# Optimization experiments

Measured on AMD Instinct MI355X. Metric: run time of the kernel, lower is better.

## Reference

```python
import jax, jax.numpy as jnp
import numpy as np

B, C, N, K = 2, 128, 8192, 16
DL = 128  # dim_L; Fourier half-dim = 64; mlp hidden = 32


def setup_inputs() -> dict:
    key = jax.random.key(0)
    ks = jax.random.split(key, 16)
    s = 0.05
    return {
        "x": jax.random.normal(ks[0], (B, C, N, 1), jnp.float32),
        "coords": jax.random.normal(ks[1], (B, N, 4), jnp.float32),
        "idx": jax.random.randint(ks[2], (B, N, K), 0, N, jnp.int64),
        "B_gauss": jax.random.normal(ks[3], (4, DL // 2), jnp.float32),
        "W1": jax.random.normal(ks[4], (DL, DL // 4), jnp.float32) * s,
        "b1": jax.random.normal(ks[5], (DL // 4,), jnp.float32) * s,
        "W2": jax.random.normal(ks[6], (DL // 4, C), jnp.float32) * s,
        "b2": jax.random.normal(ks[7], (C,), jnp.float32) * s,
        "Wq": jax.random.normal(ks[8], (C, C), jnp.float32) * s,
        "bq": jax.random.normal(ks[9], (C,), jnp.float32) * s,
        "Wk": jax.random.normal(ks[10], (C, C), jnp.float32) * s,
        "bk": jax.random.normal(ks[11], (C,), jnp.float32) * s,
        "Wv": jax.random.normal(ks[12], (C, C), jnp.float32) * s,
        "bv": jax.random.normal(ks[13], (C,), jnp.float32) * s,
        "Wo": jax.random.normal(ks[14], (C, C), jnp.float32) * s,
        "bo": jax.random.normal(ks[15], (C,), jnp.float32) * s,
    }


def reference(x, coords, idx, B_gauss, W1, b1, W2, b2, Wq, bq, Wk, bk, Wv, bv, Wo, bo):
    xs = x[..., 0]  # [B, C, N]
    # gather neighbor coords/features via KNN idx (vmapped over batch)
    nb_coords = jax.vmap(lambda c, i: c[i])(coords, idx)          # [B, N, K, 4]
    nb_feats = jax.vmap(lambda f, i: f[:, i])(xs, idx)            # [B, C, N, K]
    delta_p = nb_coords - coords[:, :, None, :]                   # [B, N, K, 4]
    # random-Fourier geometric embedding
    proj = jnp.matmul(delta_p, B_gauss)                           # [B, N, K, DL/2]
    two_pi = 2.0 * jnp.pi
    E_freq = jnp.concatenate([jnp.sin(two_pi * proj), jnp.cos(two_pi * proj)], axis=-1)
    h = jax.nn.relu(E_freq @ W1 + b1) @ W2 + b2                   # [B, N, K, C]
    E_geo = jnp.transpose(h, (0, 3, 1, 2))                        # [B, C, N, K]
    # 1x1 conv projections == channel matmuls (PyTorch conv weight acts as out<-in)
    Q = jnp.einsum('oc,bcn->bon', Wq, xs) + bq[None, :, None]     # [B, C, N]
    KV_in = nb_feats + E_geo                                      # [B, C, N, K]
    Kt = jnp.einsum('oc,bcnk->bonk', Wk, KV_in) + bk[None, :, None, None]
    Vt = jnp.einsum('oc,bcnk->bonk', Wv, KV_in) + bv[None, :, None, None]
    # local dot-product attention over K neighbors
    attn = jnp.sum(Q[..., None] * Kt, axis=1, keepdims=True) / jnp.sqrt(jnp.float32(C))
    attn = jax.nn.softmax(attn, axis=-1)                          # [B, 1, N, K]
    out = jnp.sum(attn * Vt, axis=-1, keepdims=True)              # [B, C, N, 1]
    out = jnp.einsum('oc,bcnk->bonk', Wo, out) + bo[None, :, None, None]
    return out
```

## Files before the change

### kernel.cpp

```cpp
#include <hip/hip_runtime.h>


using u16 = unsigned short;
using u32 = unsigned int;
using u64 = unsigned long long;

typedef short bf16x8 __attribute__((ext_vector_type(8)));
typedef float f32x4  __attribute__((ext_vector_type(4)));

__device__ __forceinline__ float bl(u32 u) { return __uint_as_float(u << 16); }
__device__ __forceinline__ float bh(u32 u) { return __uint_as_float(u & 0xffff0000u); }
__device__ __forceinline__ float b2f(u16 u) { return __uint_as_float(((u32)u) << 16); }
__device__ __forceinline__ u16 f2b(float f) {
    u32 u = __float_as_uint(f);
    u32 r = u + 0x7fffu + ((u >> 16) & 1u);
    return (u16)(r >> 16);
}
__device__ __forceinline__ float dot8(uint4 wv, const float* xp) {
    float4 a = *(const float4*)xp;
    float4 b = *(const float4*)(xp + 4);
    return bl(wv.x)*a.x + bh(wv.x)*a.y + bl(wv.y)*a.z + bh(wv.y)*a.w
         + bl(wv.z)*b.x + bh(wv.z)*b.y + bl(wv.w)*b.z + bh(wv.w)*b.w;
}
__device__ __forceinline__ u64 pack4(float a, float b, float c, float d) {
    return (u64)f2b(a) | ((u64)f2b(b) << 16) | ((u64)f2b(c) << 32) | ((u64)f2b(d) << 48);
}
__device__ __forceinline__ int fidxA(int m, int c) {
    return (((m >> 4)*4 + (c >> 5))*64 + ((c >> 3) & 3)*16 + (m & 15))*8 + (c & 7);
}

__global__ void __launch_bounds__(512)
k_pt(const float* __restrict__ x,
     const float* __restrict__ Wq, const float* __restrict__ bq,
     const float* __restrict__ Wk, const float* __restrict__ bk,
     const float* __restrict__ Wv, const float* __restrict__ bv,
     const float* __restrict__ Wo, const float* __restrict__ bo,
     const float* __restrict__ W1, const float* __restrict__ W2,
     const float* __restrict__ b2,
     u16* __restrict__ Afrag, u16* __restrict__ Wovfrag,
     u16* __restrict__ W1frag, u16* __restrict__ W2frag,
     u16* __restrict__ Wovt2frag,
     float* __restrict__ bA, float* __restrict__ su2,
     float* __restrict__ bov2, float* __restrict__ d0b,
     u16* __restrict__ xT)
{
    const int blk = blockIdx.x, tid = threadIdx.x;

    if (blk >= 130) {
        __shared__ u16 tile[32][33];
        const int blk2 = blk - 130;
        const int b  = blk2 >> 10;
        const int ct = (blk2 >> 8) & 3;
        const int nt = blk2 & 255;
        const int tx = tid & 31, ty = tid >> 5;
        const size_t xb = (size_t)b * 128 * 8192;
        #pragma unroll
        for (int j = 0; j < 2; ++j) {
            int c = ct*32 + ty + j*16;
            tile[ty + j*16][tx] = f2b(x[xb + (size_t)c * 8192 + (size_t)(nt*32 + tx)]);
        }
        __syncthreads();
        #pragma unroll
        for (int j = 0; j < 2; ++j) {
            int n = nt*32 + ty + j*16;
            xT[xb + (size_t)n * 128 + (size_t)(ct*32 + tx)] = tile[tx][ty + j*16];
        }
        return;
    }

    const int i = tid & 127, p = tid >> 7;
    if (blk < 128) {
        __shared__ float sWk[128], sWo[128];
        __shared__ float s_pA[4][128], s_pV[4][128];
        __shared__ float s_row[128];
        if (tid < 128) sWk[tid] = Wk[tid*128 + blk];
        else if (tid < 256) sWo[tid-128] = Wo[blk*128 + (tid-128)];
        __syncthreads();
        float accA = 0.f, accV = 0.f;
        #pragma unroll 8
        for (int o = p*32; o < p*32 + 32; ++o) {
            accA += sWk[o] * Wq[o*128 + i];
            accV += sWo[o] * Wv[o*128 + i];
        }
        s_pA[p][i] = accA; s_pV[p][i] = accV;
        __syncthreads();
        if (tid < 128) {
            float v = s_pA[0][tid] + s_pA[1][tid] + s_pA[2][tid] + s_pA[3][tid];
            Afrag[fidxA(blk, tid)] = f2b(v);
        } else if (tid < 256) {
            int ii = tid - 128;
            float v = s_pV[0][ii] + s_pV[1][ii] + s_pV[2][ii] + s_pV[3][ii];
            Wovfrag[fidxA(blk, ii)] = f2b(v);
            s_row[ii] = v;
        }
        __syncthreads();
        if (tid < 32) {
            float wv2 = 0.f;
            for (int c = 0; c < 128; ++c) wv2 += s_row[c] * W2[tid*128 + c];
            Wovt2frag[(((blk >> 4)*64) + (tid >> 3)*16 + (blk & 15))*8 + (tid & 7)] = f2b(wv2);
        } else if (tid == 32) {
            float rb2 = 0.f, a3 = 0.f;
            for (int c = 0; c < 128; ++c) rb2 += s_row[c] * b2[c];
            for (int o = 0; o < 128; ++o) a3 += sWo[o] * bv[o];
            bov2[blk] = rb2 + a3 + bo[blk];
        }
    } else if (blk == 128) {
        __shared__ float s_t[128];
        __shared__ float s_p1[4][128], s_p2[4][128];
        if (tid < 128) {
            float tt = 0.f;
            for (int c = 0; c < 128; ++c) tt += Wk[tid*128 + c] * b2[c];
            s_t[tid] = tt + bk[tid];
        }
        __syncthreads();
        float a1 = 0.f, a2 = 0.f;
        #pragma unroll 8
        for (int o = p*32; o < p*32 + 32; ++o) {
            a1 += Wk[o*128 + i] * bq[o];
            a2 += Wq[o*128 + i] * s_t[o];
        }
        s_p1[p][i] = a1; s_p2[p][i] = a2;
        __syncthreads();
        if (tid < 128) {
            bA[tid] = s_p1[0][tid] + s_p1[1][tid] + s_p1[2][tid] + s_p1[3][tid];
        } else if (tid < 256) {
            int ii = tid - 128;
            su2[ii] = s_p2[0][ii] + s_p2[1][ii] + s_p2[2][ii] + s_p2[3][ii];
        } else if (tid < 320) {
            int l = tid - 256;
            float part = bq[l]*s_t[l] + bq[l+64]*s_t[l+64];
            part += __shfl_xor(part, 1);
            part += __shfl_xor(part, 2);
            part += __shfl_xor(part, 4);
            part += __shfl_xor(part, 8);
            part += __shfl_xor(part, 16);
            part += __shfl_xor(part, 32);
            if (l == 0) *d0b = part;
        }
    } else {
        for (int e = tid; e < 4096; e += 512) {
            int ii = e & 127, r2 = e >> 7;
            {
                int nt = r2 >> 4, lmm = r2 & 15;
                int ks = ii >> 5, q = (ii >> 3) & 3, j = ii & 7;
                W1frag[((nt*4 + ks)*64 + q*16 + lmm)*8 + j] = f2b(W1[ii*32 + r2]);
            }
            {
                int mt = r2 >> 4, lmm = r2 & 15;
                int ks = ii >> 5, q = (ii >> 3) & 3, j = ii & 7;
                W2frag[((mt*4 + ks)*64 + q*16 + lmm)*8 + j] = f2b(W2[r2*128 + ii]);
            }
        }
    }
}

__global__ void __launch_bounds__(256)
k_main(const u16* __restrict__ xT, const float* __restrict__ coords,
       const int* __restrict__ idx, const float* __restrict__ Bg,
       const float* __restrict__ b1g,
       const u16* __restrict__ Afrag, const u16* __restrict__ Wovfrag,
       const u16* __restrict__ W1frag, const u16* __restrict__ W2frag,
       const u16* __restrict__ Wovt2frag,
       const float* __restrict__ bAg, const float* __restrict__ su2g,
       const float* __restrict__ bov2g, const float* __restrict__ d0bg,
       float* __restrict__ out)
{
    __shared__ __align__(16) u16   sH[128][84];
    __shared__ __align__(16) u16   s_qkb[8][136];
    __shared__ __align__(16) u16   s_gb[8][40];
    __shared__ __align__(16) u16   s_xb[8][136];
    __shared__ __align__(16) u16   sHbarT[8][40];
    __shared__ float s_attn[8][17];
    __shared__ float s_e0[8];
    __shared__ __align__(16) float sBgT[64][4];
    __shared__ int s_idx[128];

    const int tid = threadIdx.x;
    const int w = tid >> 6, l = tid & 63, lm = l & 15, lq = l >> 4, lmm = lm & 7;
    const int bsel = blockIdx.x & 1;
    const int n0 = (blockIdx.x >> 1) * 8;
    const int g0 = (bsel << 13) + n0;
    const size_t bbase = ((size_t)bsel) << 13;
    const float inv_sqrtC = 0.08838834764831845f;

    sBgT[tid >> 2][tid & 3] = Bg[(tid & 3)*64 + (tid >> 2)];
    const float c_d0b = *d0bg;

    const int r0 = (w*2)*16 + lm, r1 = (w*2 + 1)*16 + lm;
    const int j0 = idx[(size_t)g0*16 + r0];
    const int j1 = idx[(size_t)g0*16 + r1];
    if (lq == 0) { s_idx[r0] = j0; s_idx[r1] = j1; }
    float4 dA, dB;
    {
        float4 cj0 = *(const float4*)&coords[(size_t)(bbase + j0)*4];
        float4 cn0 = *(const float4*)&coords[(size_t)(g0 + w*2)*4];
        dA = make_float4(cj0.x-cn0.x, cj0.y-cn0.y, cj0.z-cn0.z, cj0.w-cn0.w);
        float4 cj1 = *(const float4*)&coords[(size_t)(bbase + j1)*4];
        float4 cn1 = *(const float4*)&coords[(size_t)(g0 + w*2 + 1)*4];
        dB = make_float4(cj1.x-cn1.x, cj1.y-cn1.y, cj1.z-cn1.z, cj1.w-cn1.w);
    }
    f32x4 accq[2] = {{0.f,0.f,0.f,0.f},{0.f,0.f,0.f,0.f}};
    {
        const bf16x8* Af = (const bf16x8*)Afrag;
        bf16x8 bfr[4];
        #pragma unroll
        for (int ks = 0; ks < 4; ++ks)
            bfr[ks] = *(const bf16x8*)&xT[(((size_t)(g0 + lmm)) << 7) + ks*32 + lq*8];
        #pragma unroll
        for (int mi = 0; mi < 2; ++mi) {
            const int ct = w*2 + mi;
            #pragma unroll
            for (int ks = 0; ks < 4; ++ks)
                accq[mi] = __builtin_amdgcn_mfma_f32_16x16x32_bf16(Af[(ct*4 + ks)*64 + l], bfr[ks], accq[mi], 0, 0, 0);
        }
    }
    if (tid >= 128 && tid < 192) {
        int t = tid - 128, n = t >> 3, sub = t & 7, c0 = sub*16;
        uint4 x0 = *(const uint4*)&xT[(((size_t)(g0 + n)) << 7) + c0];
        uint4 x1 = *(const uint4*)&xT[(((size_t)(g0 + n)) << 7) + c0 + 8];
        float part = dot8(x0, &su2g[c0]) + dot8(x1, &su2g[c0+8]);
        part += __shfl_xor(part, 1);
        part += __shfl_xor(part, 2);
        part += __shfl_xor(part, 4);
        if (sub == 0) s_e0[n] = part + c_d0b;
    }
    if (lm < 8) {
        #pragma unroll
        for (int mi = 0; mi < 2; ++mi) {
            int c0 = (w*2 + mi)*16 + lq*4;
            float4 bA4 = *(const float4*)&bAg[c0];
            *(u64*)&s_qkb[lm][c0] = pack4(accq[mi][0] + bA4.x, accq[mi][1] + bA4.y,
                                          accq[mi][2] + bA4.z, accq[mi][3] + bA4.w);
        }
    }
    __syncthreads();

    {
        const bf16x8* W1f = (const bf16x8*)W1frag;
        bf16x8 w1f[2][4];
        #pragma unroll
        for (int nt = 0; nt < 2; ++nt)
            #pragma unroll
            for (int ks = 0; ks < 4; ++ks) w1f[nt][ks] = W1f[(nt*4 + ks)*64 + l];
        const float b1a = b1g[lm], b1b = b1g[16 + lm];
        #pragma unroll
        for (int mi = 0; mi < 2; ++mi) {
            const int mt = w*2 + mi;
            float4 d = mi ? dB : dA;
            bf16x8 ea[4];
            #pragma unroll
            for (int ksp = 0; ksp < 2; ++ksp) {
                #pragma unroll
                for (int jp = 0; jp < 4; ++jp) {
                    int f = ksp*32 + lq*8 + jp*2;
                    float4 ga = *(const float4*)sBgT[f];
                    float4 gb = *(const float4*)sBgT[f+1];
                    float p0 = d.x*ga.x + d.y*ga.y + d.z*ga.z + d.w*ga.w;
                    float p1 = d.x*gb.x + d.y*gb.y + d.z*gb.z + d.w*gb.w;
                    p0 -= floorf(p0); p1 -= floorf(p1);
                    ((u32*)&ea[ksp])[jp]   = (u32)f2b(__builtin_amdgcn_sinf(p0))
                                           | ((u32)f2b(__builtin_amdgcn_sinf(p1)) << 16);
                    ((u32*)&ea[ksp+2])[jp] = (u32)f2b(__builtin_amdgcn_cosf(p0))
                                           | ((u32)f2b(__builtin_amdgcn_cosf(p1)) << 16);
                }
            }
            f32x4 acch[2] = {{0.f,0.f,0.f,0.f},{0.f,0.f,0.f,0.f}};
            #pragma unroll
            for (int ks = 0; ks < 4; ++ks) {
                acch[0] = __builtin_amdgcn_mfma_f32_16x16x32_bf16(ea[ks], w1f[0][ks], acch[0], 0,0,0);
                acch[1] = __builtin_amdgcn_mfma_f32_16x16x32_bf16(ea[ks], w1f[1][ks], acch[1], 0,0,0);
            }
            #pragma unroll
            for (int r = 0; r < 4; ++r) {
                sH[mt*16 + lq*4 + r][lm]      = f2b(fmaxf(acch[0][r] + b1a, 0.f));
                sH[mt*16 + lq*4 + r][16 + lm] = f2b(fmaxf(acch[1][r] + b1b, 0.f));
            }
        }
    }
    if (w < 2) {
        const bf16x8* W2f = (const bf16x8*)W2frag;
        f32x4 accg = {0.f,0.f,0.f,0.f};
        #pragma unroll
        for (int ks = 0; ks < 4; ++ks) {
            bf16x8 bv = *(const bf16x8*)&s_qkb[lmm][ks*32 + lq*8];
            accg = __builtin_amdgcn_mfma_f32_16x16x32_bf16(W2f[(w*4 + ks)*64 + l], bv, accg, 0, 0, 0);
        }
        if (lm < 8) {
            int m0 = w*16 + lq*4;
            *(u64*)&s_gb[lm][m0] = pack4(accg[0], accg[1], accg[2], accg[3]);
        }
    }
    __syncthreads();

    {
        bf16x8 bq4[5];
        #pragma unroll
        for (int ks = 0; ks < 4; ++ks) bq4[ks] = *(const bf16x8*)&s_qkb[lmm][ks*32 + lq*8];
        bq4[4] = *(const bf16x8*)&s_gb[lmm][lq*8];
        #pragma unroll
        for (int mi = 0; mi < 2; ++mi) {
            const int mt = w*2 + mi;
            const size_t rb = ((size_t)(bbase + (mi ? j1 : j0))) << 7;
            f32x4 acc = {0.f,0.f,0.f,0.f};
            #pragma unroll
            for (int ks = 0; ks < 4; ++ks) {
                bf16x8 a = *(const bf16x8*)&xT[rb + ks*32 + lq*8];
                acc = __builtin_amdgcn_mfma_f32_16x16x32_bf16(a, bq4[ks], acc, 0, 0, 0);
            }
            {
                bf16x8 a = *(const bf16x8*)&sH[mt*16 + lm][lq*8];
                acc = __builtin_amdgcn_mfma_f32_16x16x32_bf16(a, bq4[4], acc, 0, 0, 0);
            }
            float e0v = s_e0[mt];
            float s0 = (acc[0] + e0v) * inv_sqrtC;
            float s1 = (acc[1] + e0v) * inv_sqrtC;
            float s2 = (acc[2] + e0v) * inv_sqrtC;
            float s3 = (acc[3] + e0v) * inv_sqrtC;
            float mx = fmaxf(fmaxf(s0, s1), fmaxf(s2, s3));
            mx = fmaxf(mx, __shfl_xor(mx, 16));
            mx = fmaxf(mx, __shfl_xor(mx, 32));
            float e0_ = __expf(s0 - mx), e1_ = __expf(s1 - mx);
            float e2_ = __expf(s2 - mx), e3_ = __expf(s3 - mx);
            float sm = e0_ + e1_ + e2_ + e3_;
            sm += __shfl_xor(sm, 16);
            sm += __shfl_xor(sm, 32);
            if (lm == mt) {
                float inv = 1.f / sm;
                s_attn[mt][lq*4 + 0] = e0_ * inv;
                s_attn[mt][lq*4 + 1] = e1_ * inv;
                s_attn[mt][lq*4 + 2] = e2_ * inv;
                s_attn[mt][lq*4 + 3] = e3_ * inv;
            }
        }
    }
    __syncthreads();

    {
        int n = tid >> 5, cs = tid & 31, c0 = cs*4;
        float a0[16];
        #pragma unroll
        for (int k = 0; k < 16; ++k) a0[k] = s_attn[n][k];
        float4 facc = make_float4(0.f, 0.f, 0.f, 0.f);
        #pragma unroll
        for (int k = 0; k < 16; ++k) {
            uint2 v = *(const uint2*)&xT[(((size_t)(bbase + s_idx[n*16 + k])) << 7) + c0];
            facc.x += a0[k]*bl(v.x); facc.y += a0[k]*bh(v.x);
            facc.z += a0[k]*bl(v.y); facc.w += a0[k]*bh(v.y);
        }
        *(u64*)&s_xb[n][c0] = pack4(facc.x, facc.y, facc.z, facc.w);
        float hacc = 0.f;
        #pragma unroll
        for (int k = 0; k < 16; ++k) hacc += a0[k] * b2f(sH[n*16 + k][cs]);
        sHbarT[n][cs] = f2b(hacc);
    }
    __syncthreads();

    {
        const bf16x8* Wvf  = (const bf16x8*)Wovfrag;
        const bf16x8* Wt2f = (const bf16x8*)Wovt2frag;
        bf16x8 bx[4];
        #pragma unroll
        for (int ks = 0; ks < 4; ++ks) bx[ks] = *(const bf16x8*)&s_xb[lmm][ks*32 + lq*8];
        bf16x8 bh8 = *(const bf16x8*)&sHbarT[lmm][lq*8];
        #pragma unroll
        for (int mi = 0; mi < 2; ++mi) {
            const int ct = w*2 + mi;
            f32x4 acco = {0.f,0.f,0.f,0.f};
            #pragma unroll
            for (int ks = 0; ks < 4; ++ks)
                acco = __builtin_amdgcn_mfma_f32_16x16x32_bf16(Wvf[(ct*4 + ks)*64 + l], bx[ks], acco, 0, 0, 0);
            acco = __builtin_amdgcn_mfma_f32_16x16x32_bf16(Wt2f[ct*64 + l], bh8, acco, 0, 0, 0);
            if (lm < 8) {
                float4 bo4 = *(const float4*)&bov2g[ct*16 + lq*4];
                const float* bo4p = &bo4.x;
                #pragma unroll
                for (int r = 0; r < 4; ++r) {
                    int o = ct*16 + lq*4 + r;
                    out[(((size_t)(bsel*128 + o)) << 13) + n0 + lm] = acco[r] + bo4p[r];
                }
            }
        }
    }
}

extern "C" void kernel_launch(void* const* d_in, const int* in_sizes, int n_in,
                              void* d_out, int out_size, void* d_ws, size_t ws_size,
                              hipStream_t stream)
{
    const float* x      = (const float*)d_in[0];
    const float* coords = (const float*)d_in[1];
    const int*   idx    = (const int*)d_in[2];
    const float* Bg     = (const float*)d_in[3];
    const float* W1     = (const float*)d_in[4];
    const float* b1     = (const float*)d_in[5];
    const float* W2     = (const float*)d_in[6];
    const float* b2     = (const float*)d_in[7];
    const float* Wq     = (const float*)d_in[8];
    const float* bq     = (const float*)d_in[9];
    const float* Wk     = (const float*)d_in[10];
    const float* bk     = (const float*)d_in[11];
    const float* Wv     = (const float*)d_in[12];
    const float* bv     = (const float*)d_in[13];
    const float* Wo     = (const float*)d_in[14];
    const float* bo     = (const float*)d_in[15];
    float* out = (float*)d_out;

    char* ws = (char*)d_ws;
    u16*   Afrag    = (u16*)(ws);
    u16*   Wovfrag  = (u16*)(ws + 32768);
    u16*   W1frag   = (u16*)(ws + 65536);
    u16*   W2frag   = (u16*)(ws + 73728);
    u16*   Wovt2frag= (u16*)(ws + 81920);
    float* bA       = (float*)(ws + 90112);
    float* su2      = (float*)(ws + 90624);
    float* bov2     = (float*)(ws + 91136);
    float* d0b      = (float*)(ws + 91648);
    u16*   xT       = (u16*)(ws + 94208);

    k_pt<<<2178, 512, 0, stream>>>(x, Wq, bq, Wk, bk, Wv, bv, Wo, bo, W1, W2, b2,
                                   Afrag, Wovfrag, W1frag, W2frag, Wovt2frag,
                                   bA, su2, bov2, d0b, xT);
    k_main<<<2048, 256, 0, stream>>>(xT, coords, idx, Bg, b1,
                                     Afrag, Wovfrag, W1frag, W2frag, Wovt2frag,
                                     bA, su2, bov2, d0b, out);
}
```

Before: 142.3 us.

## Give each wavefront its own 8-point group to drop block-wide barriers

Before, four waves cooperated on one 8-point group and had to sync four times per block. Now each wave processes its own 8-point group end to end, with per-wave shared-memory slices, so every __syncthreads is removed and the launch shrinks from 2048 to 512 blocks. Each wave now does all eight m-tiles of the MFMA work serially, and shared memory per block grows roughly fourfold. That can lower occupancy and cuts the number of blocks available to fill the GPU.

```diff
diff --git a/kernel.cpp b/kernel.cpp
--- a/kernel.cpp
+++ b/kernel.cpp
@@ -165,41 +165,42 @@
        const float* __restrict__ bov2g, const float* __restrict__ d0bg,
        float* __restrict__ out)
 {
-    __shared__ __align__(16) u16   sH[128][84];
-    __shared__ __align__(16) u16   s_qkb[8][136];
-    __shared__ __align__(16) u16   s_gb[8][40];
-    __shared__ __align__(16) u16   s_xb[8][136];
-    __shared__ __align__(16) u16   sHbarT[8][40];
-    __shared__ float s_attn[8][17];
-    __shared__ float s_e0[8];
-    __shared__ __align__(16) float sBgT[64][4];
-    __shared__ int s_idx[128];
+    __shared__ __align__(16) u16   sH[4][128][40];
+    __shared__ __align__(16) float s_del[4][128][4];
+    __shared__ int   s_idx[4][128];
+    __shared__ __align__(16) u16   s_qkb[4][8][136];
+    __shared__ __align__(16) u16   s_xb[4][8][136];
+    __shared__ __align__(16) u16   s_gb[4][8][40];
+    __shared__ __align__(16) u16   s_hbt[4][8][40];
+    __shared__ float s_attn[4][8][20];
+    __shared__ float s_e0[4][8];
+    __shared__ __align__(16) float sBgT[4][64][4];
 
     const int tid = threadIdx.x;
     const int w = tid >> 6, l = tid & 63, lm = l & 15, lq = l >> 4, lmm = lm & 7;
-    const int bsel = blockIdx.x & 1;
-    const int n0 = (blockIdx.x >> 1) * 8;
-    const int g0 = (bsel << 13) + n0;
+    const int g = blockIdx.x*4 + w;
+    const int g0 = g * 8;
+    const int bsel = g0 >> 13;
+    const int n0 = g0 & 8191;
     const size_t bbase = ((size_t)bsel) << 13;
     const float inv_sqrtC = 0.08838834764831845f;
 
-    sBgT[tid >> 2][tid & 3] = Bg[(tid & 3)*64 + (tid >> 2)];
+    {
+        float4 bg;
+        bg.x = Bg[l]; bg.y = Bg[64 + l]; bg.z = Bg[128 + l]; bg.w = Bg[192 + l];
+        *(float4*)sBgT[w][l] = bg;
+    }
     const float c_d0b = *d0bg;
 
-    const int r0 = (w*2)*16 + lm, r1 = (w*2 + 1)*16 + lm;
-    const int j0 = idx[(size_t)g0*16 + r0];
-    const int j1 = idx[(size_t)g0*16 + r1];
-    if (lq == 0) { s_idx[r0] = j0; s_idx[r1] = j1; }
-    float4 dA, dB;
-    {
-        float4 cj0 = *(const float4*)&coords[(size_t)(bbase + j0)*4];
-        float4 cn0 = *(const float4*)&coords[(size_t)(g0 + w*2)*4];
-        dA = make_float4(cj0.x-cn0.x, cj0.y-cn0.y, cj0.z-cn0.z, cj0.w-cn0.w);
-        float4 cj1 = *(const float4*)&coords[(size_t)(bbase + j1)*4];
-        float4 cn1 = *(const float4*)&coords[(size_t)(g0 + w*2 + 1)*4];
-        dB = make_float4(cj1.x-cn1.x, cj1.y-cn1.y, cj1.z-cn1.z, cj1.w-cn1.w);
-    }
-    f32x4 accq[2] = {{0.f,0.f,0.f,0.f},{0.f,0.f,0.f,0.f}};
+    #pragma unroll
+    for (int h = 0; h < 2; ++h) {
+        int r = h*64 + l;
+        int j = idx[(size_t)g0*16 + r];
+        s_idx[w][r] = j;
+        float4 cj = *(const float4*)&coords[(size_t)(bbase + j)*4];
+        float4 cn = *(const float4*)&coords[(size_t)(g0 + (r >> 4))*4];
+        *(float4*)s_del[w][r] = make_float4(cj.x-cn.x, cj.y-cn.y, cj.z-cn.z, cj.w-cn.w);
+    }
     {
         const bf16x8* Af = (const bf16x8*)Afrag;
         bf16x8 bfr[4];
@@ -207,33 +208,29 @@
         for (int ks = 0; ks < 4; ++ks)
             bfr[ks] = *(const bf16x8*)&xT[(((size_t)(g0 + lmm)) << 7) + ks*32 + lq*8];
         #pragma unroll
-        for (int mi = 0; mi < 2; ++mi) {
-            const int ct = w*2 + mi;
+        for (int mt = 0; mt < 8; ++mt) {
+            f32x4 acc = {0.f,0.f,0.f,0.f};
             #pragma unroll
             for (int ks = 0; ks < 4; ++ks)
-                accq[mi] = __builtin_amdgcn_mfma_f32_16x16x32_bf16(Af[(ct*4 + ks)*64 + l], bfr[ks], accq[mi], 0, 0, 0);
-        }
-    }
-    if (tid >= 128 && tid < 192) {
-        int t = tid - 128, n = t >> 3, sub = t & 7, c0 = sub*16;
+                acc = __builtin_amdgcn_mfma_f32_16x16x32_bf16(Af[(mt*4 + ks)*64 + l], bfr[ks], acc, 0, 0, 0);
+            if (lm < 8) {
+                int c0 = mt*16 + lq*4;
+                float4 bA4 = *(const float4*)&bAg[c0];
+                *(u64*)&s_qkb[w][lm][c0] = pack4(acc[0] + bA4.x, acc[1] + bA4.y,
+                                                 acc[2] + bA4.z, acc[3] + bA4.w);
+            }
+        }
+    }
+    {
+        int n = l >> 3, sub = l & 7, c0 = sub*16;
         uint4 x0 = *(const uint4*)&xT[(((size_t)(g0 + n)) << 7) + c0];
         uint4 x1 = *(const uint4*)&xT[(((size_t)(g0 + n)) << 7) + c0 + 8];
         float part = dot8(x0, &su2g[c0]) + dot8(x1, &su2g[c0+8]);
         part += __shfl_xor(part, 1);
         part += __shfl_xor(part, 2);
         part += __shfl_xor(part, 4);
-        if (sub == 0) s_e0[n] = part + c_d0b;
-    }
-    if (lm < 8) {
-        #pragma unroll
-        for (int mi = 0; mi < 2; ++mi) {
-            int c0 = (w*2 + mi)*16 + lq*4;
-            float4 bA4 = *(const float4*)&bAg[c0];
-            *(u64*)&s_qkb[lm][c0] = pack4(accq[mi][0] + bA4.x, accq[mi][1] + bA4.y,
-                                          accq[mi][2] + bA4.z, accq[mi][3] + bA4.w);
-        }
-    }
-    __syncthreads();
+        if (sub == 0) s_e0[w][n] = part + c_d0b;
+    }
 
     {
         const bf16x8* W1f = (const bf16x8*)W1frag;
@@ -244,17 +241,16 @@
             for (int ks = 0; ks < 4; ++ks) w1f[nt][ks] = W1f[(nt*4 + ks)*64 + l];
         const float b1a = b1g[lm], b1b = b1g[16 + lm];
         #pragma unroll
-        for (int mi = 0; mi < 2; ++mi) {
-            const int mt = w*2 + mi;
-            float4 d = mi ? dB : dA;
+        for (int mt = 0; mt < 8; ++mt) {
+            float4 d = *(const float4*)s_del[w][mt*16 + lm];
             bf16x8 ea[4];
             #pragma unroll
             for (int ksp = 0; ksp < 2; ++ksp) {
                 #pragma unroll
                 for (int jp = 0; jp < 4; ++jp) {
                     int f = ksp*32 + lq*8 + jp*2;
-                    float4 ga = *(const float4*)sBgT[f];
-                    float4 gb = *(const float4*)sBgT[f+1];
+                    float4 ga = *(const float4*)sBgT[w][f];
+                    float4 gb = *(const float4*)sBgT[w][f+1];
                     float p0 = d.x*ga.x + d.y*ga.y + d.z*ga.z + d.w*ga.w;
                     float p1 = d.x*gb.x + d.y*gb.y + d.z*gb.z + d.w*gb.w;
                     p0 -= floorf(p0); p1 -= floorf(p1);
@@ -272,35 +268,35 @@
             }
             #pragma unroll
             for (int r = 0; r < 4; ++r) {
-                sH[mt*16 + lq*4 + r][lm]      = f2b(fmaxf(acch[0][r] + b1a, 0.f));
-                sH[mt*16 + lq*4 + r][16 + lm] = f2b(fmaxf(acch[1][r] + b1b, 0.f));
-            }
-        }
-    }
-    if (w < 2) {
+                sH[w][mt*16 + lq*4 + r][lm]      = f2b(fmaxf(acch[0][r] + b1a, 0.f));
+                sH[w][mt*16 + lq*4 + r][16 + lm] = f2b(fmaxf(acch[1][r] + b1b, 0.f));
+            }
+        }
         const bf16x8* W2f = (const bf16x8*)W2frag;
-        f32x4 accg = {0.f,0.f,0.f,0.f};
-        #pragma unroll
-        for (int ks = 0; ks < 4; ++ks) {
-            bf16x8 bv = *(const bf16x8*)&s_qkb[lmm][ks*32 + lq*8];
-            accg = __builtin_amdgcn_mfma_f32_16x16x32_bf16(W2f[(w*4 + ks)*64 + l], bv, accg, 0, 0, 0);
-        }
-        if (lm < 8) {
-            int m0 = w*16 + lq*4;
-            *(u64*)&s_gb[lm][m0] = pack4(accg[0], accg[1], accg[2], accg[3]);
-        }
-    }
-    __syncthreads();
+        #pragma unroll
+        for (int mt2 = 0; mt2 < 2; ++mt2) {
+            f32x4 accg = {0.f,0.f,0.f,0.f};
+            #pragma unroll
+            for (int ks = 0; ks < 4; ++ks) {
+                bf16x8 bv = *(const bf16x8*)&s_qkb[w][lmm][ks*32 + lq*8];
+                accg = __builtin_amdgcn_mfma_f32_16x16x32_bf16(W2f[(mt2*4 + ks)*64 + l], bv, accg, 0, 0, 0);
+            }
+            if (lm < 8) {
+                int m0 = mt2*16 + lq*4;
+                *(u64*)&s_gb[w][lm][m0] = pack4(accg[0], accg[1], accg[2], accg[3]);
+            }
+        }
+    }
 
     {
         bf16x8 bq4[5];
         #pragma unroll
-        for (int ks = 0; ks < 4; ++ks) bq4[ks] = *(const bf16x8*)&s_qkb[lmm][ks*32 + lq*8];
-        bq4[4] = *(const bf16x8*)&s_gb[lmm][lq*8];
-        #pragma unroll
-        for (int mi = 0; mi < 2; ++mi) {
-            const int mt = w*2 + mi;
-            const size_t rb = ((size_t)(bbase + (mi ? j1 : j0))) << 7;
+        for (int ks = 0; ks < 4; ++ks) bq4[ks] = *(const bf16x8*)&s_qkb[w][lmm][ks*32 + lq*8];
+        bq4[4] = *(const bf16x8*)&s_gb[w][lmm][lq*8];
+        #pragma unroll
+        for (int mt = 0; mt < 8; ++mt) {
+            const int j2 = s_idx[w][mt*16 + lm];
+            const size_t rb = ((size_t)(bbase + j2)) << 7;
             f32x4 acc = {0.f,0.f,0.f,0.f};
             #pragma unroll
             for (int ks = 0; ks < 4; ++ks) {
@@ -308,10 +304,10 @@
                 acc = __builtin_amdgcn_mfma_f32_16x16x32_bf16(a, bq4[ks], acc, 0, 0, 0);
             }
             {
-                bf16x8 a = *(const bf16x8*)&sH[mt*16 + lm][lq*8];
+                bf16x8 a = *(const bf16x8*)&sH[w][mt*16 + lm][lq*8];
                 acc = __builtin_amdgcn_mfma_f32_16x16x32_bf16(a, bq4[4], acc, 0, 0, 0);
             }
-            float e0v = s_e0[mt];
+            float e0v = s_e0[w][mt];
             float s0 = (acc[0] + e0v) * inv_sqrtC;
             float s1 = (acc[1] + e0v) * inv_sqrtC;
             float s2 = (acc[2] + e0v) * inv_sqrtC;
@@ -326,57 +322,68 @@
             sm += __shfl_xor(sm, 32);
             if (lm == mt) {
                 float inv = 1.f / sm;
-                s_attn[mt][lq*4 + 0] = e0_ * inv;
-                s_attn[mt][lq*4 + 1] = e1_ * inv;
-                s_attn[mt][lq*4 + 2] = e2_ * inv;
-                s_attn[mt][lq*4 + 3] = e3_ * inv;
-            }
-        }
-    }
-    __syncthreads();
-
-    {
-        int n = tid >> 5, cs = tid & 31, c0 = cs*4;
+                s_attn[w][mt][lq*4 + 0] = e0_ * inv;
+                s_attn[w][mt][lq*4 + 1] = e1_ * inv;
+                s_attn[w][mt][lq*4 + 2] = e2_ * inv;
+                s_attn[w][mt][lq*4 + 3] = e3_ * inv;
+            }
+        }
+    }
+
+    {
+        const int n = l >> 3, sub = l & 7, c0 = sub*16;
         float a0[16];
         #pragma unroll
-        for (int k = 0; k < 16; ++k) a0[k] = s_attn[n][k];
-        float4 facc = make_float4(0.f, 0.f, 0.f, 0.f);
+        for (int k = 0; k < 16; ++k) a0[k] = s_attn[w][n][k];
+        float4 f0 = {0,0,0,0}, f1 = {0,0,0,0}, f2 = {0,0,0,0}, f3 = {0,0,0,0};
         #pragma unroll
         for (int k = 0; k < 16; ++k) {
-            uint2 v = *(const uint2*)&xT[(((size_t)(bbase + s_idx[n*16 + k])) << 7) + c0];
-            facc.x += a0[k]*bl(v.x); facc.y += a0[k]*bh(v.x);
-            facc.z += a0[k]*bl(v.y); facc.w += a0[k]*bh(v.y);
-        }
-        *(u64*)&s_xb[n][c0] = pack4(facc.x, facc.y, facc.z, facc.w);
-        float hacc = 0.f;
-        #pragma unroll
-        for (int k = 0; k < 16; ++k) hacc += a0[k] * b2f(sH[n*16 + k][cs]);
-        sHbarT[n][cs] = f2b(hacc);
-    }
-    __syncthreads();
+            const size_t rb = ((size_t)(bbase + s_idx[w][n*16 + k])) << 7;
+            uint4 v0 = *(const uint4*)&xT[rb + c0];
+            uint4 v1 = *(const uint4*)&xT[rb + c0 + 8];
+            float a = a0[k];
+            f0.x += a*bl(v0.x); f0.y += a*bh(v0.x); f0.z += a*bl(v0.y); f0.w += a*bh(v0.y);
+            f1.x += a*bl(v0.z); f1.y += a*bh(v0.z); f1.z += a*bl(v0.w); f1.w += a*bh(v0.w);
+            f2.x += a*bl(v1.x); f2.y += a*bh(v1.x); f2.z += a*bl(v1.y); f2.w += a*bh(v1.y);
+            f3.x += a*bl(v1.z); f3.y += a*bh(v1.z); f3.z += a*bl(v1.w); f3.w += a*bh(v1.w);
+        }
+        *(u64*)&s_xb[w][n][c0]      = pack4(f0.x, f0.y, f0.z, f0.w);
+        *(u64*)&s_xb[w][n][c0 + 4]  = pack4(f1.x, f1.y, f1.z, f1.w);
+        *(u64*)&s_xb[w][n][c0 + 8]  = pack4(f2.x, f2.y, f2.z, f2.w);
+        *(u64*)&s_xb[w][n][c0 + 12] = pack4(f3.x, f3.y, f3.z, f3.w);
+        const int m0 = sub*4;
+        float h0 = 0.f, h1 = 0.f, h2 = 0.f, h3 = 0.f;
+        #pragma unroll
+        for (int k = 0; k < 16; ++k) {
+            const u16* hr = &sH[w][n*16 + k][m0];
+            float a = a0[k];
+            h0 += a * b2f(hr[0]); h1 += a * b2f(hr[1]);
+            h2 += a * b2f(hr[2]); h3 += a * b2f(hr[3]);
+        }
+        *(u64*)&s_hbt[w][n][m0] = pack4(h0, h1, h2, h3);
+    }
 
     {
         const bf16x8* Wvf  = (const bf16x8*)Wovfrag;
         const bf16x8* Wt2f = (const bf16x8*)Wovt2frag;
         bf16x8 bx[4];
         #pragma unroll
-        for (int ks = 0; ks < 4; ++ks) bx[ks] = *(const bf16x8*)&s_xb[lmm][ks*32 + lq*8];
-        bf16x8 bh8 = *(const bf16x8*)&sHbarT[lmm][lq*8];
-        #pragma unroll
-        for (int mi = 0; mi < 2; ++mi) {
-            const int ct = w*2 + mi;
-            f32x4 acco = {0.f,0.f,0.f,0.f};
+        for (int ks = 0; ks < 4; ++ks) bx[ks] = *(const bf16x8*)&s_xb[w][lmm][ks*32 + lq*8];
+        bf16x8 bh8 = *(const bf16x8*)&s_hbt[w][lmm][lq*8];
+        #pragma unroll
+        for (int mt = 0; mt < 8; ++mt) {
+            f32x4 acc = {0.f,0.f,0.f,0.f};
             #pragma unroll
             for (int ks = 0; ks < 4; ++ks)
-                acco = __builtin_amdgcn_mfma_f32_16x16x32_bf16(Wvf[(ct*4 + ks)*64 + l], bx[ks], acco, 0, 0, 0);
-            acco = __builtin_amdgcn_mfma_f32_16x16x32_bf16(Wt2f[ct*64 + l], bh8, acco, 0, 0, 0);
+                acc = __builtin_amdgcn_mfma_f32_16x16x32_bf16(Wvf[(mt*4 + ks)*64 + l], bx[ks], acc, 0, 0, 0);
+            acc = __builtin_amdgcn_mfma_f32_16x16x32_bf16(Wt2f[mt*64 + l], bh8, acc, 0, 0, 0);
             if (lm < 8) {
-                float4 bo4 = *(const float4*)&bov2g[ct*16 + lq*4];
+                float4 bo4 = *(const float4*)&bov2g[mt*16 + lq*4];
                 const float* bo4p = &bo4.x;
                 #pragma unroll
                 for (int r = 0; r < 4; ++r) {
-                    int o = ct*16 + lq*4 + r;
-                    out[(((size_t)(bsel*128 + o)) << 13) + n0 + lm] = acco[r] + bo4p[r];
+                    int o = mt*16 + lq*4 + r;
+                    out[(((size_t)(bsel*128 + o)) << 13) + n0 + lm] = acc[r] + bo4p[r];
                 }
             }
         }
@@ -420,7 +427,7 @@
     k_pt<<<2178, 512, 0, stream>>>(x, Wq, bq, Wk, bk, Wv, bv, Wo, bo, W1, W2, b2,
                                    Afrag, Wovfrag, W1frag, W2frag, Wovt2frag,
                                    bA, su2, bov2, d0b, xT);
-    k_main<<<2048, 256, 0, stream>>>(xT, coords, idx, Bg, b1,
-                                     Afrag, Wovfrag, W1frag, W2frag, Wovt2frag,
-                                     bA, su2, bov2, d0b, out);
-}
+    k_main<<<512, 256, 0, stream>>>(xT, coords, idx, Bg, b1,
+                                    Afrag, Wovfrag, W1frag, W2frag, Wovt2frag,
+                                    bA, su2, bov2, d0b, out);
+}
```

Result: slower. 153.4 us (+7.8%).
